# Kernel tuning notes

Hardware: AMD Instinct MI355X
Metric: run time of the kernel (lower is better)

## Reference

```python
import jax, jax.numpy as jnp
import numpy as np

N, R, B, H, C, E = 4096, 8, 30, 64, 16, 131072


def setup_inputs() -> dict:
    key = jax.random.key(0)
    ks = jax.random.split(key, 11)
    s = 0.02  # small init scale for weights
    return {
        "x": jax.random.normal(ks[0], (N, N), jnp.float32),
        "edge_index": jax.random.randint(ks[1], (2, E), 0, N, jnp.int32),
        "edge_type": jax.random.randint(ks[2], (E,), 0, R, jnp.int32),
        "basis1": jax.random.normal(ks[3], (B, N, H), jnp.float32) * s,
        "att1": jax.random.normal(ks[4], (R, B), jnp.float32) * s,
        "root1": jax.random.normal(ks[5], (N, H), jnp.float32) * s,
        "bias1": jnp.zeros((H,), jnp.float32),
        "basis2": jax.random.normal(ks[6], (B, H, C), jnp.float32) * s,
        "att2": jax.random.normal(ks[7], (R, B), jnp.float32) * s,
        "root2": jax.random.normal(ks[8], (H, C), jnp.float32) * s,
        "bias2": jnp.zeros((C,), jnp.float32),
    }


def _rgcn_conv(x, src, dst, etype, deg_inv, basis, att, root, bias):
    # Basis-decomposed relation weights: W_r = sum_b att[r,b] * basis[b]
    W = jnp.einsum("rb,bio->rio", att, basis)            # [R, in, out]
    # Pre-transform every node by every relation weight (equivalent to
    # per-edge bmm(x_j, W[edge_type]) but avoids gathering [E, in] features).
    h = jnp.einsum("ni,rio->nro", x, W)                  # [N, R, out]
    msg = h[src, etype]                                  # [E, out] per-edge message
    agg = jax.ops.segment_sum(msg, dst, num_segments=N)  # scatter-add to dst
    agg = agg * deg_inv[:, None]                         # scatter-mean (aggr='mean')
    return agg + x @ root + bias                         # root/self transform + bias


def reference(x, edge_index, edge_type, basis1, att1, root1, bias1,
              basis2, att2, root2, bias2):
    src, dst = edge_index[0], edge_index[1]
    deg = jax.ops.segment_sum(jnp.ones((E,), jnp.float32), dst, num_segments=N)
    deg_inv = 1.0 / jnp.maximum(deg, 1.0)  # zero in-degree -> 0 output, as scatter_mean
    h = jax.nn.relu(_rgcn_conv(x, src, dst, edge_type, deg_inv,
                               basis1, att1, root1, bias1))
    out = _rgcn_conv(h, src, dst, edge_type, deg_inv,
                     basis2, att2, root2, bias2)
    return jax.nn.log_softmax(out, axis=1)
```

## Files before the change

### kernel.cpp

```cpp
#include <hip/hip_runtime.h>
#include <cstdint>

#define E_CNT 131072
#define N_CNT 4096

typedef short bf16x8 __attribute__((ext_vector_type(8)));
typedef float f32x4 __attribute__((ext_vector_type(4)));

__device__ __forceinline__ ushort f2bf(float f) {
  union { float f; unsigned u; } v; v.f = f;
  unsigned r = v.u + 0x7FFFu + ((v.u >> 16) & 1u);
  return (ushort)(r >> 16);
}

__global__ __launch_bounds__(256) void k_prep(const float* __restrict__ att1,
                                              const float* __restrict__ basis1,
                                              const float* __restrict__ root1,
                                              ushort* __restrict__ wt1,
                                              const int* __restrict__ dstp,
                                              int* __restrict__ deg,
                                              const float4* __restrict__ x,
                                              ushort* __restrict__ xbf) {
  __shared__ float sT[32 * 33];
  int bid = blockIdx.x, t = threadIdx.x;
  if (bid < 256) {
    int i0 = (bid >> 1) * 32, o0 = (bid & 1) * 32;
    int ol = t & 31, ir = t >> 5;
    float a[8][4] = {};
    for (int b = 0; b < 30; b += 2) {
      float v0[4], v1[4];
#pragma unroll
      for (int k = 0; k < 4; ++k) {
        size_t ofs = (size_t)(i0 + ir + k * 8) * 64 + o0 + ol;
        v0[k] = basis1[(size_t)b * 262144 + ofs];
        v1[k] = basis1[(size_t)(b + 1) * 262144 + ofs];
      }
#pragma unroll
      for (int r = 0; r < 8; ++r) {
        float w0 = att1[r * 30 + b], w1 = att1[r * 30 + b + 1];
#pragma unroll
        for (int k = 0; k < 4; ++k) a[r][k] += w0 * v0[k] + w1 * v1[k];
      }
    }
    for (int r = 0; r < 8; ++r) {
#pragma unroll
      for (int k = 0; k < 4; ++k) sT[ol * 33 + ir + k * 8] = a[r][k];
      __syncthreads();
#pragma unroll
      for (int k = 0; k < 4; ++k) {
        int orow = ir + k * 8, icol = ol;
        wt1[(size_t)(r * 64 + o0 + orow) * 4096 + i0 + icol] = f2bf(sT[orow * 33 + icol]);
      }
      __syncthreads();
    }
  } else if (bid < 384) {
    int bb = bid - 256;
    int i0 = bb * 32;
    int ol = t & 31, ir = t >> 5;
    for (int oh = 0; oh < 2; ++oh) {
      int o0 = oh * 32;
#pragma unroll
      for (int k = 0; k < 4; ++k)
        sT[ol * 33 + ir + k * 8] = root1[(size_t)(i0 + ir + k * 8) * 64 + o0 + ol];
      __syncthreads();
#pragma unroll
      for (int k = 0; k < 4; ++k) {
        int orow = ir + k * 8, icol = ol;
        wt1[(size_t)(512 + o0 + orow) * 4096 + i0 + icol] = f2bf(sT[orow * 33 + icol]);
      }
      __syncthreads();
    }
  } else if (bid < 896) {
    int e = (bid - 384) * 256 + t;
    atomicAdd(&deg[dstp[e]], 1);
  } else {
    int i = (bid - 896) * 256 + t;
    float4 v0 = x[i * 2], v1 = x[i * 2 + 1];
    ushort o[8];
    o[0] = f2bf(v0.x); o[1] = f2bf(v0.y); o[2] = f2bf(v0.z); o[3] = f2bf(v0.w);
    o[4] = f2bf(v1.x); o[5] = f2bf(v1.y); o[6] = f2bf(v1.z); o[7] = f2bf(v1.w);
    *(ulonglong2*)(xbf + (size_t)i * 8) = *(const ulonglong2*)o;
  }
}

__global__ __launch_bounds__(1024) void k_scan(const int* __restrict__ deg,
                                               int* __restrict__ rowptr,
                                               int* __restrict__ cursor,
                                               float* __restrict__ dinv) {
  __shared__ int part[1024];
  int t = threadIdx.x;
  int base = t * 4;
  int d0 = deg[base], d1 = deg[base + 1], d2 = deg[base + 2], d3 = deg[base + 3];
  int s = d0 + d1 + d2 + d3;
  part[t] = s;
  __syncthreads();
  for (int off = 1; off < 1024; off <<= 1) {
    int v = part[t];
    int u = (t >= off) ? part[t - off] : 0;
    __syncthreads();
    part[t] = v + u;
    __syncthreads();
  }
  int incl = part[t];
  int excl = incl - s;
  int p0 = excl, p1 = excl + d0, p2 = p1 + d1, p3 = p2 + d2;
  rowptr[base] = p0; rowptr[base + 1] = p1; rowptr[base + 2] = p2; rowptr[base + 3] = p3;
  cursor[base] = p0; cursor[base + 1] = p1; cursor[base + 2] = p2; cursor[base + 3] = p3;
  dinv[base]     = 1.0f / fmaxf((float)d0, 1.0f);
  dinv[base + 1] = 1.0f / fmaxf((float)d1, 1.0f);
  dinv[base + 2] = 1.0f / fmaxf((float)d2, 1.0f);
  dinv[base + 3] = 1.0f / fmaxf((float)d3, 1.0f);
  if (t == 1023) rowptr[4096] = incl;
}

__global__ __launch_bounds__(256) void k_mid(const int* __restrict__ srcp,
                                             const int* __restrict__ dstp,
                                             const int* __restrict__ et,
                                             int* __restrict__ cursor,
                                             int* __restrict__ spack,
                                             const float* __restrict__ att2,
                                             const float* __restrict__ basis2,
                                             const float* __restrict__ root2,
                                             float* __restrict__ w2e) {
  int bid = blockIdx.x, t = threadIdx.x;
  if (bid < 512) {
    int e = bid * 256 + t;
    int d = dstp[e];
    int pos = atomicAdd(&cursor[d], 1);
    spack[pos] = (srcp[e] << 3) | et[e];
  } else {
    int r = bid - 512;
    for (int q = t; q < 1024; q += 256) {
      float a = 0.f;
      if (r < 8) {
        for (int b = 0; b < 30; ++b) a += att2[r * 30 + b] * basis2[b * 1024 + q];
      } else {
        a = root2[q];
      }
      w2e[r * 1024 + q] = a;
    }
  }
}

__global__ __launch_bounds__(256, 3) void k_gemm1(const ushort* __restrict__ xbf,
                                                  const ushort* __restrict__ wt1,
                                                  float* __restrict__ c1) {
  __shared__ __align__(16) ushort As[128 * 128];
  __shared__ __align__(16) ushort Bs[64 * 128];
  int bid = blockIdx.x;
  int swz = (bid & 7) * 144 + (bid >> 3);
  int kp = swz / 288, rem = swz % 288;
  int bm = rem / 9, bn = rem % 9;
  int m0 = bm * 128, n0 = bn * 64, kbase = kp * 1024;
  int tid = threadIdx.x;
  int lane = tid & 63, wid = tid >> 6;
  int wm = wid >> 1, wn = wid & 1;

  f32x4 acc[4][2] = {};

  for (int tt = 0; tt < 8; ++tt) {
    int k0 = kbase + tt * 128;
#pragma unroll
    for (int it = 0; it < 8; ++it) {
      int flat = it * 256 + tid;
      int row = flat >> 4, gg = flat & 15;
      int gcol = k0 + ((gg ^ (row & 7)) << 3);
      const ushort* g = xbf + (size_t)(m0 + row) * 4096 + gcol;
      ushort* l = &As[(it * 256 + wid * 64) * 8];
      __builtin_amdgcn_global_load_lds((const __attribute__((address_space(1))) void*)g,
                                       (__attribute__((address_space(3))) void*)l, 16, 0, 0);
    }
#pragma unroll
    for (int it = 0; it < 4; ++it) {
      int flat = it * 256 + tid;
      int row = flat >> 4, gg = flat & 15;
      int gcol = k0 + ((gg ^ (row & 7)) << 3);
      const ushort* g = wt1 + (size_t)(n0 + row) * 4096 + gcol;
      ushort* l = &Bs[(it * 256 + wid * 64) * 8];
      __builtin_amdgcn_global_load_lds((const __attribute__((address_space(1))) void*)g,
                                       (__attribute__((address_space(3))) void*)l, 16, 0, 0);
    }
    __syncthreads();
    int q = lane >> 4, sw = lane & 7, r16 = lane & 15;
#pragma unroll
    for (int ks = 0; ks < 4; ++ks) {
      int co = ((ks * 4 + q) ^ sw) << 3;
      bf16x8 b0 = *(const bf16x8*)&Bs[(wn * 32 + 0 * 16 + r16) * 128 + co];
      bf16x8 b1 = *(const bf16x8*)&Bs[(wn * 32 + 1 * 16 + r16) * 128 + co];
      bf16x8 a0 = *(const bf16x8*)&As[(wm * 64 + 0 * 16 + r16) * 128 + co];
      bf16x8 a1 = *(const bf16x8*)&As[(wm * 64 + 1 * 16 + r16) * 128 + co];
      bf16x8 a2 = *(const bf16x8*)&As[(wm * 64 + 2 * 16 + r16) * 128 + co];
      bf16x8 a3 = *(const bf16x8*)&As[(wm * 64 + 3 * 16 + r16) * 128 + co];
      __builtin_amdgcn_s_setprio(1);
      acc[0][0] = __builtin_amdgcn_mfma_f32_16x16x32_bf16(a0, b0, acc[0][0], 0, 0, 0);
      acc[0][1] = __builtin_amdgcn_mfma_f32_16x16x32_bf16(a0, b1, acc[0][1], 0, 0, 0);
      acc[1][0] = __builtin_amdgcn_mfma_f32_16x16x32_bf16(a1, b0, acc[1][0], 0, 0, 0);
      acc[1][1] = __builtin_amdgcn_mfma_f32_16x16x32_bf16(a1, b1, acc[1][1], 0, 0, 0);
      acc[2][0] = __builtin_amdgcn_mfma_f32_16x16x32_bf16(a2, b0, acc[2][0], 0, 0, 0);
      acc[2][1] = __builtin_amdgcn_mfma_f32_16x16x32_bf16(a2, b1, acc[2][1], 0, 0, 0);
      acc[3][0] = __builtin_amdgcn_mfma_f32_16x16x32_bf16(a3, b0, acc[3][0], 0, 0, 0);
      acc[3][1] = __builtin_amdgcn_mfma_f32_16x16x32_bf16(a3, b1, acc[3][1], 0, 0, 0);
      __builtin_amdgcn_s_setprio(0);
    }
    __syncthreads();
  }

  int cf = lane & 15, rf4 = (lane >> 4) * 4;
#pragma unroll
  for (int mi = 0; mi < 4; ++mi)
#pragma unroll
    for (int ni = 0; ni < 2; ++ni) {
      int gcol = n0 + wn * 32 + ni * 16 + cf;
#pragma unroll
      for (int j = 0; j < 4; ++j) {
        int grow = m0 + wm * 64 + mi * 16 + rf4 + j;
        atomicAdd(&c1[(size_t)grow * 576 + gcol], acc[mi][ni][j]);
      }
    }
}

__global__ __launch_bounds__(256) void k_agg1h2(const float* __restrict__ c1,
                                                const int* __restrict__ rowptr,
                                                const int* __restrict__ spack,
                                                const float* __restrict__ dinv,
                                                const float* __restrict__ bias1,
                                                const float* __restrict__ w2e,
                                                float* __restrict__ h2c) {
  __shared__ float sh[4][64];
  int g = threadIdx.x >> 6, t = threadIdx.x & 63;
  int n = blockIdx.x * 4 + g;
  int s0 = rowptr[n], s1 = rowptr[n + 1];
  float acc = 0.f;
  int e = s0;
  for (; e + 3 < s1; e += 4) {
    int p0 = spack[e], p1 = spack[e + 1], p2 = spack[e + 2], p3 = spack[e + 3];
    float v0 = c1[(size_t)(p0 >> 3) * 576 + (p0 & 7) * 64 + t];
    float v1 = c1[(size_t)(p1 >> 3) * 576 + (p1 & 7) * 64 + t];
    float v2 = c1[(size_t)(p2 >> 3) * 576 + (p2 & 7) * 64 + t];
    float v3 = c1[(size_t)(p3 >> 3) * 576 + (p3 & 7) * 64 + t];
    acc += (v0 + v1) + (v2 + v3);
  }
  for (; e < s1; ++e) {
    int p = spack[e];
    acc += c1[(size_t)(p >> 3) * 576 + (p & 7) * 64 + t];
  }
  float v = acc * dinv[n] + c1[(size_t)n * 576 + 512 + t] + bias1[t];
  sh[g][t] = fmaxf(v, 0.f);
  __syncthreads();
  float* o = h2c + (size_t)n * 144;
  for (int rc = t; rc < 144; rc += 64) {
    int r9 = rc >> 4, c = rc & 15;
    const float* w = w2e + r9 * 1024 + c;
    float a = 0.f;
#pragma unroll
    for (int hh = 0; hh < 64; ++hh) a += sh[g][hh] * w[hh * 16];
    o[rc] = a;
  }
}

__global__ __launch_bounds__(64) void k_agg2(const float* __restrict__ h2c,
                                             const int* __restrict__ rowptr,
                                             const int* __restrict__ spack,
                                             const float* __restrict__ dinv,
                                             const float* __restrict__ bias2,
                                             float* __restrict__ out) {
  __shared__ float red[64];
  int n = blockIdx.x, t = threadIdx.x;
  int c = t & 15, q = t >> 4;
  int s0 = rowptr[n], s1 = rowptr[n + 1];
  float acc = 0.f;
  for (int e = s0 + q; e < s1; e += 4) {
    int p = spack[e];
    acc += h2c[(size_t)(p >> 3) * 144 + (p & 7) * 16 + c];
  }
  red[t] = acc;
  __syncthreads();
  if (t < 16) {
    float sum = red[c] + red[16 + c] + red[32 + c] + red[48 + c];
    float v = sum * dinv[n] + h2c[(size_t)n * 144 + 128 + c] + bias2[c];
    float m = v;
#pragma unroll
    for (int off = 1; off < 16; off <<= 1) m = fmaxf(m, __shfl_xor(m, off, 64));
    float ex = expf(v - m);
    float s = ex;
#pragma unroll
    for (int off = 1; off < 16; off <<= 1) s += __shfl_xor(s, off, 64);
    out[n * 16 + c] = v - m - logf(s);
  }
}

extern "C" void kernel_launch(void* const* d_in, const int* in_sizes, int n_in,
                              void* d_out, int out_size, void* d_ws, size_t ws_size,
                              hipStream_t stream) {
  const float* x      = (const float*)d_in[0];
  const int*   ei     = (const int*)d_in[1];
  const int*   et     = (const int*)d_in[2];
  const float* basis1 = (const float*)d_in[3];
  const float* att1   = (const float*)d_in[4];
  const float* root1  = (const float*)d_in[5];
  const float* bias1  = (const float*)d_in[6];
  const float* basis2 = (const float*)d_in[7];
  const float* att2   = (const float*)d_in[8];
  const float* root2  = (const float*)d_in[9];
  const float* bias2  = (const float*)d_in[10];
  float* out = (float*)d_out;

  char* ws = (char*)d_ws;
  size_t off = 0;
  auto alloc = [&](size_t bytes) {
    void* p = ws + off;
    off = (off + bytes + 255) & ~(size_t)255;
    return p;
  };
  ushort* xbf  = (ushort*)alloc((size_t)N_CNT * N_CNT * 2);
  ushort* wt1  = (ushort*)alloc((size_t)576 * 4096 * 2);
  float*  c1   = (float*)alloc((size_t)N_CNT * 576 * 4);
  float*  w2e  = (float*)alloc((size_t)9 * 64 * 16 * 4);
  float*  h2c  = (float*)alloc((size_t)N_CNT * 144 * 4);
  int*    deg    = (int*)alloc(4096 * 4);
  float*  dinv   = (float*)alloc(4096 * 4);
  int*    rowptr = (int*)alloc(4097 * 4);
  int*    cursor = (int*)alloc(4096 * 4);
  int*    spack  = (int*)alloc((size_t)E_CNT * 4);

  const int* srcp = ei;
  const int* dstp = ei + E_CNT;

  hipMemsetAsync(deg, 0, 4096 * 4, stream);
  hipMemsetAsync(c1, 0, (size_t)N_CNT * 576 * 4, stream);
  k_prep<<<9088, 256, 0, stream>>>(att1, basis1, root1, wt1, dstp, deg,
                                   (const float4*)x, xbf);
  k_scan<<<1, 1024, 0, stream>>>(deg, rowptr, cursor, dinv);
  k_mid<<<521, 256, 0, stream>>>(srcp, dstp, et, cursor, spack,
                                 att2, basis2, root2, w2e);
  k_gemm1<<<1152, 256, 0, stream>>>(xbf, wt1, c1);
  k_agg1h2<<<1024, 256, 0, stream>>>(c1, rowptr, spack, dinv, bias1, w2e, h2c);
  k_agg2<<<4096, 64, 0, stream>>>(h2c, rowptr, spack, dinv, bias2, out);
}
```

Baseline: 136.2 us.

## Replace CSR build with atomic scatter-add aggregation and shrink GEMM K-tile

Measured after the change: 140.4 us. +3.1%, slower.

```diff
diff --git a/kernel.cpp b/kernel.cpp
--- a/kernel.cpp
+++ b/kernel.cpp
@@ -19,6 +19,10 @@
                                               ushort* __restrict__ wt1,
                                               const int* __restrict__ dstp,
                                               int* __restrict__ deg,
+                                              const float* __restrict__ att2,
+                                              const float* __restrict__ basis2,
+                                              const float* __restrict__ root2,
+                                              float* __restrict__ w2e,
                                               const float4* __restrict__ x,
                                               ushort* __restrict__ xbf) {
   __shared__ float sT[32 * 33];
@@ -73,63 +77,8 @@
   } else if (bid < 896) {
     int e = (bid - 384) * 256 + t;
     atomicAdd(&deg[dstp[e]], 1);
-  } else {
-    int i = (bid - 896) * 256 + t;
-    float4 v0 = x[i * 2], v1 = x[i * 2 + 1];
-    ushort o[8];
-    o[0] = f2bf(v0.x); o[1] = f2bf(v0.y); o[2] = f2bf(v0.z); o[3] = f2bf(v0.w);
-    o[4] = f2bf(v1.x); o[5] = f2bf(v1.y); o[6] = f2bf(v1.z); o[7] = f2bf(v1.w);
-    *(ulonglong2*)(xbf + (size_t)i * 8) = *(const ulonglong2*)o;
-  }
-}
-
-__global__ __launch_bounds__(1024) void k_scan(const int* __restrict__ deg,
-                                               int* __restrict__ rowptr,
-                                               int* __restrict__ cursor,
-                                               float* __restrict__ dinv) {
-  __shared__ int part[1024];
-  int t = threadIdx.x;
-  int base = t * 4;
-  int d0 = deg[base], d1 = deg[base + 1], d2 = deg[base + 2], d3 = deg[base + 3];
-  int s = d0 + d1 + d2 + d3;
-  part[t] = s;
-  __syncthreads();
-  for (int off = 1; off < 1024; off <<= 1) {
-    int v = part[t];
-    int u = (t >= off) ? part[t - off] : 0;
-    __syncthreads();
-    part[t] = v + u;
-    __syncthreads();
-  }
-  int incl = part[t];
-  int excl = incl - s;
-  int p0 = excl, p1 = excl + d0, p2 = p1 + d1, p3 = p2 + d2;
-  rowptr[base] = p0; rowptr[base + 1] = p1; rowptr[base + 2] = p2; rowptr[base + 3] = p3;
-  cursor[base] = p0; cursor[base + 1] = p1; cursor[base + 2] = p2; cursor[base + 3] = p3;
-  dinv[base]     = 1.0f / fmaxf((float)d0, 1.0f);
-  dinv[base + 1] = 1.0f / fmaxf((float)d1, 1.0f);
-  dinv[base + 2] = 1.0f / fmaxf((float)d2, 1.0f);
-  dinv[base + 3] = 1.0f / fmaxf((float)d3, 1.0f);
-  if (t == 1023) rowptr[4096] = incl;
-}
-
-__global__ __launch_bounds__(256) void k_mid(const int* __restrict__ srcp,
-                                             const int* __restrict__ dstp,
-                                             const int* __restrict__ et,
-                                             int* __restrict__ cursor,
-                                             int* __restrict__ spack,
-                                             const float* __restrict__ att2,
-                                             const float* __restrict__ basis2,
-                                             const float* __restrict__ root2,
-                                             float* __restrict__ w2e) {
-  int bid = blockIdx.x, t = threadIdx.x;
-  if (bid < 512) {
-    int e = bid * 256 + t;
-    int d = dstp[e];
-    int pos = atomicAdd(&cursor[d], 1);
-    spack[pos] = (srcp[e] << 3) | et[e];
-  } else {
-    int r = bid - 512;
+  } else if (bid < 905) {
+    int r = bid - 896;
     for (int q = t; q < 1024; q += 256) {
       float a = 0.f;
       if (r < 8) {
@@ -139,14 +88,21 @@
       }
       w2e[r * 1024 + q] = a;
     }
-  }
-}
-
-__global__ __launch_bounds__(256, 3) void k_gemm1(const ushort* __restrict__ xbf,
+  } else {
+    int i = (bid - 905) * 256 + t;
+    float4 v0 = x[i * 2], v1 = x[i * 2 + 1];
+    ushort o[8];
+    o[0] = f2bf(v0.x); o[1] = f2bf(v0.y); o[2] = f2bf(v0.z); o[3] = f2bf(v0.w);
+    o[4] = f2bf(v1.x); o[5] = f2bf(v1.y); o[6] = f2bf(v1.z); o[7] = f2bf(v1.w);
+    *(ulonglong2*)(xbf + (size_t)i * 8) = *(const ulonglong2*)o;
+  }
+}
+
+__global__ __launch_bounds__(256, 5) void k_gemm1(const ushort* __restrict__ xbf,
                                                   const ushort* __restrict__ wt1,
                                                   float* __restrict__ c1) {
-  __shared__ __align__(16) ushort As[128 * 128];
-  __shared__ __align__(16) ushort Bs[64 * 128];
+  __shared__ __align__(16) ushort As[128 * 64];
+  __shared__ __align__(16) ushort Bs[64 * 64];
   int bid = blockIdx.x;
   int swz = (bid & 7) * 144 + (bid >> 3);
   int kp = swz / 288, rem = swz % 288;
@@ -158,12 +114,12 @@
 
   f32x4 acc[4][2] = {};
 
-  for (int tt = 0; tt < 8; ++tt) {
-    int k0 = kbase + tt * 128;
-#pragma unroll
-    for (int it = 0; it < 8; ++it) {
+  for (int tt = 0; tt < 16; ++tt) {
+    int k0 = kbase + tt * 64;
+#pragma unroll
+    for (int it = 0; it < 4; ++it) {
       int flat = it * 256 + tid;
-      int row = flat >> 4, gg = flat & 15;
+      int row = flat >> 3, gg = flat & 7;
       int gcol = k0 + ((gg ^ (row & 7)) << 3);
       const ushort* g = xbf + (size_t)(m0 + row) * 4096 + gcol;
       ushort* l = &As[(it * 256 + wid * 64) * 8];
@@ -171,9 +127,9 @@
                                        (__attribute__((address_space(3))) void*)l, 16, 0, 0);
     }
 #pragma unroll
-    for (int it = 0; it < 4; ++it) {
+    for (int it = 0; it < 2; ++it) {
       int flat = it * 256 + tid;
-      int row = flat >> 4, gg = flat & 15;
+      int row = flat >> 3, gg = flat & 7;
       int gcol = k0 + ((gg ^ (row & 7)) << 3);
       const ushort* g = wt1 + (size_t)(n0 + row) * 4096 + gcol;
       ushort* l = &Bs[(it * 256 + wid * 64) * 8];
@@ -183,14 +139,14 @@
     __syncthreads();
     int q = lane >> 4, sw = lane & 7, r16 = lane & 15;
 #pragma unroll
-    for (int ks = 0; ks < 4; ++ks) {
+    for (int ks = 0; ks < 2; ++ks) {
       int co = ((ks * 4 + q) ^ sw) << 3;
-      bf16x8 b0 = *(const bf16x8*)&Bs[(wn * 32 + 0 * 16 + r16) * 128 + co];
-      bf16x8 b1 = *(const bf16x8*)&Bs[(wn * 32 + 1 * 16 + r16) * 128 + co];
-      bf16x8 a0 = *(const bf16x8*)&As[(wm * 64 + 0 * 16 + r16) * 128 + co];
-      bf16x8 a1 = *(const bf16x8*)&As[(wm * 64 + 1 * 16 + r16) * 128 + co];
-      bf16x8 a2 = *(const bf16x8*)&As[(wm * 64 + 2 * 16 + r16) * 128 + co];
-      bf16x8 a3 = *(const bf16x8*)&As[(wm * 64 + 3 * 16 + r16) * 128 + co];
+      bf16x8 b0 = *(const bf16x8*)&Bs[(wn * 32 + 0 * 16 + r16) * 64 + co];
+      bf16x8 b1 = *(const bf16x8*)&Bs[(wn * 32 + 1 * 16 + r16) * 64 + co];
+      bf16x8 a0 = *(const bf16x8*)&As[(wm * 64 + 0 * 16 + r16) * 64 + co];
+      bf16x8 a1 = *(const bf16x8*)&As[(wm * 64 + 1 * 16 + r16) * 64 + co];
+      bf16x8 a2 = *(const bf16x8*)&As[(wm * 64 + 2 * 16 + r16) * 64 + co];
+      bf16x8 a3 = *(const bf16x8*)&As[(wm * 64 + 3 * 16 + r16) * 64 + co];
       __builtin_amdgcn_s_setprio(1);
       acc[0][0] = __builtin_amdgcn_mfma_f32_16x16x32_bf16(a0, b0, acc[0][0], 0, 0, 0);
       acc[0][1] = __builtin_amdgcn_mfma_f32_16x16x32_bf16(a0, b1, acc[0][1], 0, 0, 0);
@@ -219,32 +175,33 @@
     }
 }
 
-__global__ __launch_bounds__(256) void k_agg1h2(const float* __restrict__ c1,
-                                                const int* __restrict__ rowptr,
-                                                const int* __restrict__ spack,
-                                                const float* __restrict__ dinv,
-                                                const float* __restrict__ bias1,
-                                                const float* __restrict__ w2e,
-                                                float* __restrict__ h2c) {
+__global__ __launch_bounds__(256) void k_sc1(const int* __restrict__ srcp,
+                                             const int* __restrict__ dstp,
+                                             const int* __restrict__ et,
+                                             const float* __restrict__ c1,
+                                             float* __restrict__ agg) {
+  int wv = (blockIdx.x * 256 + threadIdx.x) >> 6;
+  int lane = threadIdx.x & 63;
+  int e0 = wv * 16;
+#pragma unroll 4
+  for (int e = e0; e < e0 + 16; ++e) {
+    int s = srcp[e], d = dstp[e], r = et[e];
+    float v = c1[(size_t)s * 576 + r * 64 + lane];
+    atomicAdd(&agg[(size_t)d * 64 + lane], v);
+  }
+}
+
+__global__ __launch_bounds__(256) void k_h(const float* __restrict__ agg,
+                                           const int* __restrict__ deg,
+                                           const float* __restrict__ c1,
+                                           const float* __restrict__ bias1,
+                                           const float* __restrict__ w2e,
+                                           float* __restrict__ h2c) {
   __shared__ float sh[4][64];
   int g = threadIdx.x >> 6, t = threadIdx.x & 63;
   int n = blockIdx.x * 4 + g;
-  int s0 = rowptr[n], s1 = rowptr[n + 1];
-  float acc = 0.f;
-  int e = s0;
-  for (; e + 3 < s1; e += 4) {
-    int p0 = spack[e], p1 = spack[e + 1], p2 = spack[e + 2], p3 = spack[e + 3];
-    float v0 = c1[(size_t)(p0 >> 3) * 576 + (p0 & 7) * 64 + t];
-    float v1 = c1[(size_t)(p1 >> 3) * 576 + (p1 & 7) * 64 + t];
-    float v2 = c1[(size_t)(p2 >> 3) * 576 + (p2 & 7) * 64 + t];
-    float v3 = c1[(size_t)(p3 >> 3) * 576 + (p3 & 7) * 64 + t];
-    acc += (v0 + v1) + (v2 + v3);
-  }
-  for (; e < s1; ++e) {
-    int p = spack[e];
-    acc += c1[(size_t)(p >> 3) * 576 + (p & 7) * 64 + t];
-  }
-  float v = acc * dinv[n] + c1[(size_t)n * 576 + 512 + t] + bias1[t];
+  float dinv = 1.0f / fmaxf((float)deg[n], 1.0f);
+  float v = agg[(size_t)n * 64 + t] * dinv + c1[(size_t)n * 576 + 512 + t] + bias1[t];
   sh[g][t] = fmaxf(v, 0.f);
   __syncthreads();
   float* o = h2c + (size_t)n * 144;
@@ -258,35 +215,40 @@
   }
 }
 
-__global__ __launch_bounds__(64) void k_agg2(const float* __restrict__ h2c,
-                                             const int* __restrict__ rowptr,
-                                             const int* __restrict__ spack,
-                                             const float* __restrict__ dinv,
+__global__ __launch_bounds__(256) void k_sc2(const int* __restrict__ srcp,
+                                             const int* __restrict__ dstp,
+                                             const int* __restrict__ et,
+                                             const float* __restrict__ h2c,
+                                             float* __restrict__ outagg) {
+  int wv = (blockIdx.x * 256 + threadIdx.x) >> 6;
+  int lane = threadIdx.x & 63;
+  int sub = lane >> 4, c = lane & 15;
+  int e0 = wv * 32;
+  for (int e = e0 + sub; e < e0 + 32; e += 4) {
+    int s = srcp[e], d = dstp[e], r = et[e];
+    float v = h2c[(size_t)s * 144 + r * 16 + c];
+    atomicAdd(&outagg[(size_t)d * 16 + c], v);
+  }
+}
+
+__global__ __launch_bounds__(256) void k_out(const float* __restrict__ outagg,
+                                             const int* __restrict__ deg,
+                                             const float* __restrict__ h2c,
                                              const float* __restrict__ bias2,
                                              float* __restrict__ out) {
-  __shared__ float red[64];
-  int n = blockIdx.x, t = threadIdx.x;
-  int c = t & 15, q = t >> 4;
-  int s0 = rowptr[n], s1 = rowptr[n + 1];
-  float acc = 0.f;
-  for (int e = s0 + q; e < s1; e += 4) {
-    int p = spack[e];
-    acc += h2c[(size_t)(p >> 3) * 144 + (p & 7) * 16 + c];
-  }
-  red[t] = acc;
-  __syncthreads();
-  if (t < 16) {
-    float sum = red[c] + red[16 + c] + red[32 + c] + red[48 + c];
-    float v = sum * dinv[n] + h2c[(size_t)n * 144 + 128 + c] + bias2[c];
-    float m = v;
-#pragma unroll
-    for (int off = 1; off < 16; off <<= 1) m = fmaxf(m, __shfl_xor(m, off, 64));
-    float ex = expf(v - m);
-    float s = ex;
-#pragma unroll
-    for (int off = 1; off < 16; off <<= 1) s += __shfl_xor(s, off, 64);
-    out[n * 16 + c] = v - m - logf(s);
-  }
+  int t = threadIdx.x;
+  int n = blockIdx.x * 16 + (t >> 4);
+  int c = t & 15;
+  float dinv = 1.0f / fmaxf((float)deg[n], 1.0f);
+  float v = outagg[(size_t)n * 16 + c] * dinv + h2c[(size_t)n * 144 + 128 + c] + bias2[c];
+  float m = v;
+#pragma unroll
+  for (int off = 1; off < 16; off <<= 1) m = fmaxf(m, __shfl_xor(m, off, 64));
+  float ex = expf(v - m);
+  float s = ex;
+#pragma unroll
+  for (int off = 1; off < 16; off <<= 1) s += __shfl_xor(s, off, 64);
+  out[(size_t)n * 16 + c] = v - m - logf(s);
 }
 
 extern "C" void kernel_launch(void* const* d_in, const int* in_sizes, int n_in,
@@ -312,28 +274,26 @@
     off = (off + bytes + 255) & ~(size_t)255;
     return p;
   };
-  ushort* xbf  = (ushort*)alloc((size_t)N_CNT * N_CNT * 2);
-  ushort* wt1  = (ushort*)alloc((size_t)576 * 4096 * 2);
-  float*  c1   = (float*)alloc((size_t)N_CNT * 576 * 4);
-  float*  w2e  = (float*)alloc((size_t)9 * 64 * 16 * 4);
-  float*  h2c  = (float*)alloc((size_t)N_CNT * 144 * 4);
-  int*    deg    = (int*)alloc(4096 * 4);
-  float*  dinv   = (float*)alloc(4096 * 4);
-  int*    rowptr = (int*)alloc(4097 * 4);
-  int*    cursor = (int*)alloc(4096 * 4);
-  int*    spack  = (int*)alloc((size_t)E_CNT * 4);
+  float* c1     = (float*)alloc((size_t)N_CNT * 576 * 4);
+  float* agg    = (float*)alloc((size_t)N_CNT * 64 * 4);
+  float* outagg = (float*)alloc((size_t)N_CNT * 16 * 4);
+  int*   deg    = (int*)alloc(4096 * 4);
+  size_t zbytes = off;
+  ushort* xbf = (ushort*)alloc((size_t)N_CNT * N_CNT * 2);
+  ushort* wt1 = (ushort*)alloc((size_t)576 * 4096 * 2);
+  float*  w2e = (float*)alloc((size_t)9 * 64 * 16 * 4);
+  float*  h2c = (float*)alloc((size_t)N_CNT * 144 * 4);
 
   const int* srcp = ei;
   const int* dstp = ei + E_CNT;
 
-  hipMemsetAsync(deg, 0, 4096 * 4, stream);
-  hipMemsetAsync(c1, 0, (size_t)N_CNT * 576 * 4, stream);
-  k_prep<<<9088, 256, 0, stream>>>(att1, basis1, root1, wt1, dstp, deg,
+  hipMemsetAsync(c1, 0, zbytes, stream);
+  k_prep<<<9097, 256, 0, stream>>>(att1, basis1, root1, wt1, dstp, deg,
+                                   att2, basis2, root2, w2e,
                                    (const float4*)x, xbf);
-  k_scan<<<1, 1024, 0, stream>>>(deg, rowptr, cursor, dinv);
-  k_mid<<<521, 256, 0, stream>>>(srcp, dstp, et, cursor, spack,
-                                 att2, basis2, root2, w2e);
   k_gemm1<<<1152, 256, 0, stream>>>(xbf, wt1, c1);
-  k_agg1h2<<<1024, 256, 0, stream>>>(c1, rowptr, spack, dinv, bias1, w2e, h2c);
-  k_agg2<<<4096, 64, 0, stream>>>(h2c, rowptr, spack, dinv, bias2, out);
-}
+  k_sc1<<<2048, 256, 0, stream>>>(srcp, dstp, et, c1, agg);
+  k_h<<<1024, 256, 0, stream>>>(agg, deg, c1, bias1, w2e, h2c);
+  k_sc2<<<1024, 256, 0, stream>>>(srcp, dstp, et, h2c, outagg);
+  k_out<<<256, 256, 0, stream>>>(outagg, deg, h2c, bias2, out);
+}
```
